# Kernel optimization log

Hardware: AMD Instinct MI355X
Metric: run time of the kernel (lower is better)

Reference implementation:

```python
import jax, jax.numpy as jnp
import numpy as np

N_EMBD = 1024
N_HEAD = 16
HEAD_SIZE = N_EMBD // N_HEAD  # 64
HEAD_INDEX = 0
# ALiBi slope: x = (2**8)**(1/n_head); slope = 1 / x**(head_index+1)
SLOPE = 1.0 / ((2.0 ** 8) ** (1.0 / N_HEAD)) ** (HEAD_INDEX + 1)
B, T = 4, 4096


def setup_inputs() -> dict:
    key = jax.random.key(0)
    kx, kq, kk, kv = jax.random.split(key, 4)
    x = jax.random.normal(kx, (B, T, N_EMBD), dtype=jnp.float32)
    wq = jax.random.normal(kq, (HEAD_SIZE, N_EMBD), dtype=jnp.float32) * 0.02
    wk = jax.random.normal(kk, (HEAD_SIZE, N_EMBD), dtype=jnp.float32) * 0.02
    wv = jax.random.normal(kv, (HEAD_SIZE, N_EMBD), dtype=jnp.float32) * 0.02
    return {"x": x, "wq": wq, "wk": wk, "wv": wv}


def reference(x, wq, wk, wv):
    Bq, Tq, C = x.shape
    q = jnp.einsum('btc,hc->bth', x, wq)  # [B,T,Hd]
    k = jnp.einsum('btc,hc->bth', x, wk)
    v = jnp.einsum('btc,hc->bth', x, wv)
    # NOTE: original scales by C**-0.5 where C = n_embd (full dim), not head_size
    wei = jnp.einsum('bth,bsh->bts', q, k) * (C ** -0.5)  # [B,T,T]
    idx = jnp.arange(Tq)
    distance = idx[None, :] - idx[:, None]  # [T,T], j - i
    wei = wei + distance.astype(wei.dtype) * jnp.asarray(SLOPE, wei.dtype)
    causal = distance <= 0  # tril: key index j <= query index i
    wei = jnp.where(causal[None, :, :], wei, -jnp.inf)
    wei = jax.nn.softmax(wei, axis=-1)
    out = jnp.einsum('bts,bsh->bth', wei, v)  # [B,T,Hd]
    return out
```

## Files before the change

kernel.cpp:

```cpp
#include <hip/hip_runtime.h>
#include <hip/hip_bf16.h>
#include <stdint.h>
#include <math.h>

typedef __attribute__((ext_vector_type(8))) short bf16x8;
typedef __attribute__((ext_vector_type(4))) float f32x4;

#define TSEQ 4096
#define LOG2E 1.44269504088896340736f
#define SLOPE 0.70710678118654752440f
#define SL2E (SLOPE * LOG2E)

__device__ __forceinline__ unsigned short f32_to_bf16(float f) {
  union { float f; unsigned int u; } v; v.f = f;
  unsigned int r = v.u + 0x7fffu + ((v.u >> 16) & 1u);
  return (unsigned short)(r >> 16);
}

__device__ __forceinline__ unsigned int pk2(float a, float b) {
  union { __hip_bfloat162 h; unsigned int u; } c;
  c.h = __float22bfloat162_rn(make_float2(a, b));
  return c.u;
}
__device__ __forceinline__ bf16x8 cvt8(f32x4 a, f32x4 b) {
  union { unsigned int u[4]; bf16x8 v; } r;
  r.u[0] = pk2(a[0], a[1]); r.u[1] = pk2(a[2], a[3]);
  r.u[2] = pk2(b[0], b[1]); r.u[3] = pk2(b[2], b[3]);
  return r.v;
}

__device__ __forceinline__ void async_cp16(const void* g, void* l) {
  __builtin_amdgcn_global_load_lds(
      (const __attribute__((address_space(1))) unsigned int*)g,
      (__attribute__((address_space(3))) unsigned int*)l, 16, 0, 0);
}

__global__ __launch_bounds__(256) void init_kernel(
    const float* __restrict__ wq, const float* __restrict__ wk,
    const float* __restrict__ wv, unsigned short* __restrict__ Wb) {
  int tid = blockIdx.x * 256 + threadIdx.x;
  if (tid >= 24576) return;
  int lane = tid & 63, s = (tid >> 6) & 31, nt = (tid >> 11) & 3, t = tid >> 13;
  int n = nt * 16 + (lane & 15);
  int k = s * 32 + (lane >> 4) * 8;
  const float* src = (t == 0 ? wq : (t == 1 ? wk : wv)) + (size_t)n * 1024 + k;
  f32x4 a = *(const f32x4*)src;
  f32x4 b = *(const f32x4*)(src + 4);
  if (t == 0) {
#pragma unroll
    for (int j = 0; j < 4; ++j) { a[j] *= 0.03125f; b[j] *= 0.03125f; }
  }
  *(bf16x8*)(Wb + (size_t)tid * 8) = cvt8(a, b);
}

__global__ __launch_bounds__(256, 2) void proj_kernel(
    const float* __restrict__ x, const unsigned short* __restrict__ Wb,
    unsigned short* __restrict__ qb, unsigned short* __restrict__ kb,
    unsigned short* __restrict__ vt) {
  __shared__ float xlds[4][2][16][64];
  __shared__ unsigned short wlds[4][2][6][64][8];

  const int tix = threadIdx.x;
  const int lane = tix & 63;
  const int wc = tix >> 6;
  const int l16 = lane & 15, quad = lane >> 4;
  const int R0 = blockIdx.x * 16;

  f32x4 acc0 = {0.f, 0.f, 0.f, 0.f};
  f32x4 acc1 = {0.f, 0.f, 0.f, 0.f};
  f32x4 acc2 = {0.f, 0.f, 0.f, 0.f};

  const float* xsrc[4];
#pragma unroll
  for (int c = 0; c < 4; ++c) {
    int rg = c * 4 + quad;
    int g = l16 ^ (rg & 15);
    xsrc[c] = x + (size_t)(R0 + rg) * 1024 + g * 4;
  }
  const unsigned short* wsrc[3];
#pragma unroll
  for (int cc = 0; cc < 3; ++cc)
    wsrc[cc] = Wb + ((size_t)((wc * 3 + cc) * 32) * 64 + lane) * 8;

  auto issue = [&](int s, int bi) {
#pragma unroll
    for (int c = 0; c < 4; ++c)
      async_cp16(xsrc[c] + s * 64, &xlds[wc][bi][c * 4][0]);
#pragma unroll
    for (int cc = 0; cc < 3; ++cc)
#pragma unroll
      for (int ss = 0; ss < 2; ++ss)
        async_cp16(wsrc[cc] + (size_t)(2 * s + ss) * 512,
                   &wlds[wc][bi][cc * 2 + ss][0][0]);
  };
  auto compute = [&](int bi) {
    const float* base = &xlds[wc][bi][l16][0];
#pragma unroll
    for (int ss = 0; ss < 2; ++ss) {
      f32x4 a0 = *(const f32x4*)(base + ((ss * 8 + quad * 2) ^ l16) * 4);
      f32x4 a1 = *(const f32x4*)(base + ((ss * 8 + quad * 2 + 1) ^ l16) * 4);
      bf16x8 af = cvt8(a0, a1);
      acc0 = __builtin_amdgcn_mfma_f32_16x16x32_bf16(
          af, *(const bf16x8*)&wlds[wc][bi][0 + ss][lane][0], acc0, 0, 0, 0);
      acc1 = __builtin_amdgcn_mfma_f32_16x16x32_bf16(
          af, *(const bf16x8*)&wlds[wc][bi][2 + ss][lane][0], acc1, 0, 0, 0);
      acc2 = __builtin_amdgcn_mfma_f32_16x16x32_bf16(
          af, *(const bf16x8*)&wlds[wc][bi][4 + ss][lane][0], acc2, 0, 0, 0);
    }
  };

  issue(0, 0);
  issue(1, 1);
#pragma unroll 1
  for (int s = 0; s < 16; ++s) {
    if (s < 15) asm volatile("s_waitcnt vmcnt(10)" ::: "memory");
    else        asm volatile("s_waitcnt vmcnt(0)" ::: "memory");
    __builtin_amdgcn_sched_barrier(0);
    compute(s & 1);
    __builtin_amdgcn_sched_barrier(0);
    if (s + 2 < 16) {
      asm volatile("s_waitcnt lgkmcnt(0)" ::: "memory");
      __builtin_amdgcn_sched_barrier(0);
      issue(s + 2, s & 1);
    }
    __builtin_amdgcn_sched_barrier(0);
  }

#pragma unroll
  for (int cc = 0; cc < 3; ++cc) {
    const int ci = wc * 3 + cc;
    const f32x4 a = (cc == 0) ? acc0 : (cc == 1) ? acc1 : acc2;
#pragma unroll
    for (int r = 0; r < 4; ++r) {
      int row = R0 + quad * 4 + r;
      unsigned short hv = f32_to_bf16(a[r]);
      if (ci < 4) {
        qb[(size_t)row * 64 + ci * 16 + l16] = hv;
      } else if (ci < 8) {
        kb[(size_t)row * 64 + (ci - 4) * 16 + l16] = hv;
      } else {
        int b = row >> 12, tt = row & 4095;
        vt[((size_t)b * 64 + (ci - 8) * 16 + l16) * TSEQ + tt] = hv;
      }
    }
  }
}

__global__ __launch_bounds__(64) void attn_kernel(
    const unsigned short* __restrict__ qb, const unsigned short* __restrict__ kb,
    const unsigned short* __restrict__ vt, float* __restrict__ out) {
  __shared__ unsigned short pbuf[16][40];

  const int lane = threadIdx.x & 63;
  const int l16 = lane & 15, quad = lane >> 4;
  const int tid = blockIdx.x;
  const int b = tid & 3;
  const int r0 = (tid >> 2) << 4;
  const int j0 = (r0 >= 16) ? (r0 - 16) : 0;

  const unsigned short* kbase = kb + (size_t)b * TSEQ * 64;
  const unsigned short* vbase = vt + (size_t)b * 64 * TSEQ;

  const unsigned short* qrow = qb + (size_t)(b * TSEQ + r0 + l16) * 64 + quad * 8;
  bf16x8 qa0 = *(const bf16x8*)qrow;
  bf16x8 qa1 = *(const bf16x8*)(qrow + 32);

  f32x4 o[5];
#pragma unroll
  for (int dt = 0; dt < 5; ++dt) o[dt] = (f32x4){0.f, 0.f, 0.f, 0.f};

  const int irel = j0 + l16 - r0 - quad * 4;
  const float fb = SL2E * (float)irel;

#pragma unroll
  for (int nt = 0; nt < 2; ++nt) {
    const unsigned short* krow = kbase + (size_t)(j0 + nt * 16 + l16) * 64 + quad * 8;
    f32x4 sa = (f32x4){0.f, 0.f, 0.f, 0.f};
    sa = __builtin_amdgcn_mfma_f32_16x16x32_bf16(qa0, *(const bf16x8*)krow, sa, 0, 0, 0);
    sa = __builtin_amdgcn_mfma_f32_16x16x32_bf16(qa1, *(const bf16x8*)(krow + 32), sa, 0, 0, 0);
#pragma unroll
    for (int r = 0; r < 4; ++r) {
      float arg = fmaf(sa[r], LOG2E, fb + SL2E * (float)(nt * 16 - r));
      float p = exp2f(arg);
      if (irel + nt * 16 - r > 0) p = 0.f;
      pbuf[quad * 4 + r][nt * 16 + l16] = f32_to_bf16(p);
    }
  }
  bf16x8 pa = *(const bf16x8*)&pbuf[l16][quad * 8];

#pragma unroll
  for (int dt = 0; dt < 4; ++dt) {
    const unsigned short* vrow = vbase + (size_t)(dt * 16 + l16) * TSEQ + j0 + quad * 8;
    o[dt] = __builtin_amdgcn_mfma_f32_16x16x32_bf16(pa, *(const bf16x8*)vrow, o[dt], 0, 0, 0);
  }
  {
    union { unsigned int u[4]; bf16x8 v; } ones;
    ones.u[0] = ones.u[1] = ones.u[2] = ones.u[3] = 0x3F803F80u;
    o[4] = __builtin_amdgcn_mfma_f32_16x16x32_bf16(pa, ones.v, o[4], 0, 0, 0);
  }

#pragma unroll
  for (int r = 0; r < 4; ++r) {
    const float invl = 1.0f / o[4][r];
    const int row = b * TSEQ + r0 + quad * 4 + r;
#pragma unroll
    for (int dt = 0; dt < 4; ++dt)
      out[(size_t)row * 64 + dt * 16 + l16] = o[dt][r] * invl;
  }
}

extern "C" void kernel_launch(void* const* d_in, const int* in_sizes, int n_in,
                              void* d_out, int out_size, void* d_ws, size_t ws_size,
                              hipStream_t stream) {
  const float* x  = (const float*)d_in[0];
  const float* wq = (const float*)d_in[1];
  const float* wk = (const float*)d_in[2];
  const float* wv = (const float*)d_in[3];
  float* out = (float*)d_out;

  char* ws = (char*)d_ws;
  unsigned short* Wb = (unsigned short*)(ws);
  unsigned short* qb = (unsigned short*)(ws + 393216);
  unsigned short* kb = (unsigned short*)(ws + 393216 + 2097152);
  unsigned short* vt = (unsigned short*)(ws + 393216 + 2 * 2097152);

  init_kernel<<<96, 256, 0, stream>>>(wq, wk, wv, Wb);
  proj_kernel<<<1024, 256, 0, stream>>>(x, Wb, qb, kb, vt);
  attn_kernel<<<1024, 64, 0, stream>>>(qb, kb, vt, out);
}
```

Measured before the change: 129.2 us.

## Share one LDS copy of x rows across waves and stream weights through registers

The projection kernel used to stage a private double-buffered copy of the same 16 x rows in LDS for each of its four waves, plus per-wave weight tiles. Now the block loads the full 16x1024 fp32 row tile once, cooperatively and with an XOR swizzle, into one shared LDS buffer guarded by a single barrier. Weight fragments are loaded straight into registers with ping-pong register double-buffering. The aim is to cut the redundant global and L2 traffic for x and drop the per-step LDS staging of weights. The cost is a 64KB LDS footprint per block, which may limit occupancy, and no overlap of the x load with compute.

```diff
diff --git a/kernel.cpp b/kernel.cpp
--- a/kernel.cpp
+++ b/kernel.cpp
@@ -57,8 +57,7 @@
     const float* __restrict__ x, const unsigned short* __restrict__ Wb,
     unsigned short* __restrict__ qb, unsigned short* __restrict__ kb,
     unsigned short* __restrict__ vt) {
-  __shared__ float xlds[4][2][16][64];
-  __shared__ unsigned short wlds[4][2][6][64][8];
+  __shared__ float xb[16][1024];
 
   const int tix = threadIdx.x;
   const int lane = tix & 63;
@@ -70,60 +69,54 @@
   f32x4 acc1 = {0.f, 0.f, 0.f, 0.f};
   f32x4 acc2 = {0.f, 0.f, 0.f, 0.f};
 
-  const float* xsrc[4];
-#pragma unroll
-  for (int c = 0; c < 4; ++c) {
-    int rg = c * 4 + quad;
-    int g = l16 ^ (rg & 15);
-    xsrc[c] = x + (size_t)(R0 + rg) * 1024 + g * 4;
-  }
-  const unsigned short* wsrc[3];
-#pragma unroll
-  for (int cc = 0; cc < 3; ++cc)
-    wsrc[cc] = Wb + ((size_t)((wc * 3 + cc) * 32) * 64 + lane) * 8;
-
-  auto issue = [&](int s, int bi) {
-#pragma unroll
-    for (int c = 0; c < 4; ++c)
-      async_cp16(xsrc[c] + s * 64, &xlds[wc][bi][c * 4][0]);
-#pragma unroll
-    for (int cc = 0; cc < 3; ++cc)
-#pragma unroll
-      for (int ss = 0; ss < 2; ++ss)
-        async_cp16(wsrc[cc] + (size_t)(2 * s + ss) * 512,
-                   &wlds[wc][bi][cc * 2 + ss][0][0]);
+#pragma unroll
+  for (int r4 = 0; r4 < 4; ++r4) {
+    const int row = wc * 4 + r4;
+    const float* rs = x + (size_t)(R0 + row) * 1024 + (lane ^ (row & 15)) * 4;
+#pragma unroll
+    for (int h = 0; h < 4; ++h)
+      async_cp16(rs + h * 256, &xb[row][h * 256]);
+  }
+  const unsigned short* wsrc0 = Wb + ((size_t)((wc * 3 + 0) * 32) * 64 + lane) * 8;
+  const unsigned short* wsrc1 = Wb + ((size_t)((wc * 3 + 1) * 32) * 64 + lane) * 8;
+  const unsigned short* wsrc2 = Wb + ((size_t)((wc * 3 + 2) * 32) * 64 + lane) * 8;
+
+  auto load_w = [&](int g, bf16x8 (&w)[3][4]) {
+#pragma unroll
+    for (int ss = 0; ss < 4; ++ss) {
+      const size_t o = (size_t)(4 * g + ss) * 512;
+      w[0][ss] = *(const bf16x8*)(wsrc0 + o);
+      w[1][ss] = *(const bf16x8*)(wsrc1 + o);
+      w[2][ss] = *(const bf16x8*)(wsrc2 + o);
+    }
   };
-  auto compute = [&](int bi) {
-    const float* base = &xlds[wc][bi][l16][0];
-#pragma unroll
-    for (int ss = 0; ss < 2; ++ss) {
-      f32x4 a0 = *(const f32x4*)(base + ((ss * 8 + quad * 2) ^ l16) * 4);
-      f32x4 a1 = *(const f32x4*)(base + ((ss * 8 + quad * 2 + 1) ^ l16) * 4);
+  auto compute = [&](int g, bf16x8 (&w)[3][4]) {
+#pragma unroll
+    for (int ss = 0; ss < 4; ++ss) {
+      const int c0 = (g * 4 + ss) * 8 + quad * 2;
+      f32x4 a0 = *(const f32x4*)(&xb[l16][0] + ((c0 ^ l16) * 4));
+      f32x4 a1 = *(const f32x4*)(&xb[l16][0] + (((c0 + 1) ^ l16) * 4));
       bf16x8 af = cvt8(a0, a1);
-      acc0 = __builtin_amdgcn_mfma_f32_16x16x32_bf16(
-          af, *(const bf16x8*)&wlds[wc][bi][0 + ss][lane][0], acc0, 0, 0, 0);
-      acc1 = __builtin_amdgcn_mfma_f32_16x16x32_bf16(
-          af, *(const bf16x8*)&wlds[wc][bi][2 + ss][lane][0], acc1, 0, 0, 0);
-      acc2 = __builtin_amdgcn_mfma_f32_16x16x32_bf16(
-          af, *(const bf16x8*)&wlds[wc][bi][4 + ss][lane][0], acc2, 0, 0, 0);
+      acc0 = __builtin_amdgcn_mfma_f32_16x16x32_bf16(af, w[0][ss], acc0, 0, 0, 0);
+      acc1 = __builtin_amdgcn_mfma_f32_16x16x32_bf16(af, w[1][ss], acc1, 0, 0, 0);
+      acc2 = __builtin_amdgcn_mfma_f32_16x16x32_bf16(af, w[2][ss], acc2, 0, 0, 0);
     }
   };
 
-  issue(0, 0);
-  issue(1, 1);
+  bf16x8 wA[3][4], wB[3][4];
+  load_w(0, wA);
+  __builtin_amdgcn_sched_barrier(0);
+  asm volatile("s_waitcnt vmcnt(12)" ::: "memory");
+  __builtin_amdgcn_sched_barrier(0);
+  __builtin_amdgcn_s_barrier();
+  __builtin_amdgcn_sched_barrier(0);
+
 #pragma unroll 1
-  for (int s = 0; s < 16; ++s) {
-    if (s < 15) asm volatile("s_waitcnt vmcnt(10)" ::: "memory");
-    else        asm volatile("s_waitcnt vmcnt(0)" ::: "memory");
-    __builtin_amdgcn_sched_barrier(0);
-    compute(s & 1);
-    __builtin_amdgcn_sched_barrier(0);
-    if (s + 2 < 16) {
-      asm volatile("s_waitcnt lgkmcnt(0)" ::: "memory");
-      __builtin_amdgcn_sched_barrier(0);
-      issue(s + 2, s & 1);
-    }
-    __builtin_amdgcn_sched_barrier(0);
+  for (int g = 0; g < 8; g += 2) {
+    if (g + 1 < 8) load_w(g + 1, wB);
+    compute(g, wA);
+    if (g + 2 < 8) load_w(g + 2, wA);
+    compute(g + 1, wB);
   }
 
 #pragma unroll
```

After: 115.1 us. 10.9% less time.
